# Kernel optimization log

Hardware: AMD Instinct MI355X
Metric: run time of the kernel (lower is better)

## Reference

```python
import jax, jax.numpy as jnp
import numpy as np

BATCH, SEQ, IN, HID = 64, 2048, 512, 512


def setup_inputs() -> dict:
    key = jax.random.key(0)
    ks = jax.random.split(key, 6)
    s = 1.0 / np.sqrt(HID)  # torch RNNCell uniform init scale
    return {
        "inputs": jax.random.normal(ks[0], (BATCH, SEQ, IN), dtype=jnp.float32),
        "h0": jax.random.normal(ks[1], (BATCH, HID), dtype=jnp.float32),
        "W_ih": jax.random.uniform(ks[2], (HID, IN), jnp.float32, -s, s),
        "W_hh": jax.random.uniform(ks[3], (HID, HID), jnp.float32, -s, s),
        "b_ih": jax.random.uniform(ks[4], (HID,), jnp.float32, -s, s),
        "b_hh": jax.random.uniform(ks[5], (HID,), jnp.float32, -s, s),
    }


def reference(inputs, h0, W_ih, W_hh, b_ih, b_hh):
    # hidden_state.reshape(-1, hidden_size) in the original
    h0 = h0.reshape(-1, W_hh.shape[0])
    # Precompute input projection for all timesteps in one big GEMM: [B,S,H]
    x_proj = jnp.einsum("bsi,hi->bsh", inputs, W_ih) + b_ih

    def step(h, xp_t):  # xp_t: [B,H]
        h_new = jnp.tanh(xp_t + h @ W_hh.T + b_hh)
        return h_new, h_new

    h_final, outs = jax.lax.scan(step, h0, jnp.swapaxes(x_proj, 0, 1))
    return jnp.swapaxes(outs, 0, 1), h_final  # ([B,S,H], [B,H])
```

## Files before the change

kernel.cpp:

```cpp
#include <hip/hip_runtime.h>

#define B_ 64
#define S_ 2048
#define I_ 512
#define H_ 512

typedef _Float16 half2v __attribute__((ext_vector_type(2)));
typedef _Float16 half8v __attribute__((ext_vector_type(8)));
typedef float    float4v __attribute__((ext_vector_type(4)));
typedef unsigned int uint4v __attribute__((ext_vector_type(4)));
typedef unsigned short ushort_t;

__device__ inline unsigned int pk2(float a, float b) {
    return __builtin_bit_cast(unsigned int, __builtin_amdgcn_cvt_pkrtz(a, b));
}

__device__ inline uint4v pack8(float4v a, float4v b) {
    uint4v r;
    r.x = pk2(a.x, a.y);
    r.y = pk2(a.z, a.w);
    r.z = pk2(b.x, b.y);
    r.w = pk2(b.z, b.w);
    return r;
}

__device__ inline float fdot2u(unsigned int h2, unsigned int w2, float acc) {
    return __builtin_amdgcn_fdot2(__builtin_bit_cast(half2v, h2),
                                  __builtin_bit_cast(half2v, w2), acc, false);
}

__global__ __launch_bounds__(256, 2) void xproj_gemm(
    const float* __restrict__ A,
    const float* __restrict__ Bw,
    const float* __restrict__ bias,
    float* __restrict__ C)
{
    __shared__ uint4v As[64 * 5];
    __shared__ uint4v Bs[512 * 5];

    const int tid  = threadIdx.x;
    const int wave = tid >> 6;
    const int lane = tid & 63;
    const int lm   = lane & 15;
    const int lq   = lane >> 4;
    const int m0   = blockIdx.x * 64;
    const int nb   = wave * 128;

    float4v acc[4][8];
#pragma unroll
    for (int mf = 0; mf < 4; ++mf)
#pragma unroll
        for (int nf = 0; nf < 8; ++nf)
            acc[mf][nf] = (float4v){0.f, 0.f, 0.f, 0.f};

    float biasv[8];
#pragma unroll
    for (int nf = 0; nf < 8; ++nf)
        biasv[nf] = bias[nb + nf * 16 + lm];

    const int sm    = tid >> 2;
    const int skq   = tid & 3;
    const int sslot = skq ^ (sm & 3);

    for (int kt = 0; kt < 16; ++kt) {
        const int k0 = kt * 32;
        const float* ap = A + (size_t)(m0 + sm) * 512 + k0 + skq * 8;
        float4v a0 = *(const float4v*)ap;
        float4v a1 = *(const float4v*)(ap + 4);
        float4v b0[8], b1[8];
#pragma unroll
        for (int i = 0; i < 8; ++i) {
            const float* bp = Bw + (size_t)(sm + 64 * i) * 512 + k0 + skq * 8;
            b0[i] = *(const float4v*)bp;
            b1[i] = *(const float4v*)(bp + 4);
        }
        __syncthreads();
        As[sm * 5 + sslot] = pack8(a0, a1);
#pragma unroll
        for (int i = 0; i < 8; ++i)
            Bs[(sm + 64 * i) * 5 + sslot] = pack8(b0[i], b1[i]);
        __syncthreads();

        half8v af[4];
#pragma unroll
        for (int mf = 0; mf < 4; ++mf) {
            int row = mf * 16 + lm;
            af[mf] = __builtin_bit_cast(half8v, As[row * 5 + (lq ^ (lm & 3))]);
        }
        half8v bfr[8];
#pragma unroll
        for (int nf = 0; nf < 8; ++nf) {
            int row = nb + nf * 16 + lm;
            bfr[nf] = __builtin_bit_cast(half8v, Bs[row * 5 + (lq ^ (lm & 3))]);
        }
#pragma unroll
        for (int mf = 0; mf < 4; ++mf)
#pragma unroll
            for (int nf = 0; nf < 8; ++nf)
                acc[mf][nf] = __builtin_amdgcn_mfma_f32_16x16x32_f16(
                    af[mf], bfr[nf], acc[mf][nf], 0, 0, 0);
    }

#pragma unroll
    for (int mf = 0; mf < 4; ++mf) {
        int mrow = m0 + mf * 16 + lq * 4;
#pragma unroll
        for (int nf = 0; nf < 8; ++nf) {
            float* cp = C + (size_t)mrow * 512 + nb + nf * 16 + lm;
            float4v v = acc[mf][nf];
            cp[0]    = v.x + biasv[nf];
            cp[512]  = v.y + biasv[nf];
            cp[1024] = v.z + biasv[nf];
            cp[1536] = v.w + biasv[nf];
        }
    }
}

__global__ __launch_bounds__(1024, 1) void rnn_scan(
    const float* __restrict__ h0,
    const float* __restrict__ Whh,
    const float* __restrict__ bhh,
    float* __restrict__ out)
{
    __shared__ uint4v stagev[2][64];
    __shared__ float  part[512];

    const int tid = threadIdx.x;
    const int j   = tid & 511;
    const int kh  = tid >> 9;
    const int b   = blockIdx.x;

    unsigned int w[128];
    const float* wp = Whh + (size_t)j * 512 + kh * 256;
#pragma unroll
    for (int c = 0; c < 64; ++c) {
        float4v f = *(const float4v*)(wp + c * 4);
        w[c * 2 + 0] = pk2(f.x, f.y);
        w[c * 2 + 1] = pk2(f.z, f.w);
    }

    float bj = 0.f, xpA = 0.f, xpB = 0.f;
    float* outb = out + (size_t)b * S_ * H_ + j;
    if (kh == 0) {
        ((ushort_t*)stagev)[j] = (ushort_t)pk2(h0[b * 512 + j], 0.f);
        bj  = bhh[j];
        xpA = outb[0];
        xpB = outb[512];
    }
    __syncthreads();

    for (int t = 0; t < S_; ++t) {
        const uint4v* hs = &stagev[t & 1][kh * 32];
        float a0 = 0.f, a1 = 0.f, a2 = 0.f, a3 = 0.f;
#pragma unroll
        for (int c = 0; c < 32; ++c) {
            uint4v hh = hs[c];
            a0 = fdot2u(hh.x, w[c * 4 + 0], a0);
            a1 = fdot2u(hh.y, w[c * 4 + 1], a1);
            a2 = fdot2u(hh.z, w[c * 4 + 2], a2);
            a3 = fdot2u(hh.w, w[c * 4 + 3], a3);
        }
        float a = (a0 + a1) + (a2 + a3);
        if (kh == 1) part[j] = a;
        __syncthreads();
        if (kh == 0) {
            float y = a + part[j] + ((t & 1) ? xpB : xpA) + bj;
            float e = __builtin_amdgcn_exp2f(y * 2.88539008f);
            float h = 1.f - 2.f * __builtin_amdgcn_rcpf(e + 1.f);
            outb[(size_t)t * H_] = h;
            ((ushort_t*)stagev)[((t + 1) & 1) * 512 + j] = (ushort_t)pk2(h, 0.f);
            float nxt = outb[(size_t)(t + 2) * H_];
            if (t & 1) xpB = nxt; else xpA = nxt;
            if (t == S_ - 1) out[(size_t)B_ * S_ * H_ + b * 512 + j] = h;
        }
        __syncthreads();
    }
}

extern "C" void kernel_launch(void* const* d_in, const int* in_sizes, int n_in,
                              void* d_out, int out_size, void* d_ws, size_t ws_size,
                              hipStream_t stream) {
    const float* inputs = (const float*)d_in[0];
    const float* h0     = (const float*)d_in[1];
    const float* W_ih   = (const float*)d_in[2];
    const float* W_hh   = (const float*)d_in[3];
    const float* b_ih   = (const float*)d_in[4];
    const float* b_hh   = (const float*)d_in[5];
    float* out = (float*)d_out;

    hipLaunchKernelGGL(xproj_gemm, dim3(131072 / 64), dim3(256), 0, stream,
                       inputs, W_ih, b_ih, out);
    hipLaunchKernelGGL(rnn_scan, dim3(B_), dim3(1024), 0, stream,
                       h0, W_hh, b_hh, out);
}
```

Before: 6.836 ms.

## Restructure RNN scan into per-wave row groups with DPP reductions and single barrier

Each wave now owns 32 hidden rows, and each lane holds a K-slice of 8 rows of W_hh in registers. Partial dot products are reduced across lanes with DPP adds instead of a shared-memory partial buffer. This cuts the per-step barriers from two to one and unrolls the step loop by two to ping-pong the h buffers. Only 4 of every 16 lanes apply tanh and write two outputs each, which adds cross-lane reduction cost and selection logic per step.

```diff
diff --git a/kernel.cpp b/kernel.cpp
--- a/kernel.cpp
+++ b/kernel.cpp
@@ -8,6 +8,7 @@
 typedef _Float16 half2v __attribute__((ext_vector_type(2)));
 typedef _Float16 half8v __attribute__((ext_vector_type(8)));
 typedef float    float4v __attribute__((ext_vector_type(4)));
+typedef float    float2v __attribute__((ext_vector_type(2)));
 typedef unsigned int uint4v __attribute__((ext_vector_type(4)));
 typedef unsigned short ushort_t;
 
@@ -28,6 +29,15 @@
     return __builtin_amdgcn_fdot2(__builtin_bit_cast(half2v, h2),
                                   __builtin_bit_cast(half2v, w2), acc, false);
 }
+
+__device__ inline float fast_tanh(float y) {
+    float e = __builtin_amdgcn_exp2f(y * 2.88539008f);
+    return 1.f - 2.f * __builtin_amdgcn_rcpf(e + 1.f);
+}
+
+#define DPPADD(v, ctrl)                                                       \
+    ((v) + __builtin_bit_cast(float, __builtin_amdgcn_update_dpp(             \
+               0, __builtin_bit_cast(int, (v)), (ctrl), 0xf, 0xf, true)))
 
 __global__ __launch_bounds__(256, 2) void xproj_gemm(
     const float* __restrict__ A,
@@ -122,59 +132,108 @@
     const float* __restrict__ bhh,
     float* __restrict__ out)
 {
-    __shared__ uint4v stagev[2][64];
-    __shared__ float  part[512];
-
-    const int tid = threadIdx.x;
-    const int j   = tid & 511;
-    const int kh  = tid >> 9;
-    const int b   = blockIdx.x;
-
-    unsigned int w[128];
-    const float* wp = Whh + (size_t)j * 512 + kh * 256;
-#pragma unroll
-    for (int c = 0; c < 64; ++c) {
-        float4v f = *(const float4v*)(wp + c * 4);
-        w[c * 2 + 0] = pk2(f.x, f.y);
-        w[c * 2 + 1] = pk2(f.z, f.w);
-    }
-
-    float bj = 0.f, xpA = 0.f, xpB = 0.f;
-    float* outb = out + (size_t)b * S_ * H_ + j;
-    if (kh == 0) {
-        ((ushort_t*)stagev)[j] = (ushort_t)pk2(h0[b * 512 + j], 0.f);
-        bj  = bhh[j];
-        xpA = outb[0];
-        xpB = outb[512];
-    }
+    __shared__ uint4v stage0[64];
+    __shared__ uint4v stage1[64];
+
+    const int tid   = threadIdx.x;
+    const int w     = tid >> 6;
+    const int lane  = tid & 63;
+    const int jl    = lane >> 4;
+    const int kl    = lane & 15;
+    const int b     = blockIdx.x;
+    const int wbase = w * 32;
+
+    uint4v wf[8][4];
+#pragma unroll
+    for (int q = 0; q < 8; ++q) {
+        const float* wp = Whh + (size_t)(wbase + jl * 8 + q) * 512 + kl * 8;
+#pragma unroll
+        for (int i = 0; i < 4; ++i) {
+            float4v f0 = *(const float4v*)(wp + i * 128);
+            float4v f1 = *(const float4v*)(wp + i * 128 + 4);
+            wf[q][i] = pack8(f0, f1);
+        }
+    }
+
+    float* outb = out + (size_t)b * S_ * H_;
+    const int jj = wbase + jl * 8 + 2 * kl;
+
+    float be = 0.f, bo = 0.f;
+    float xeA = 0.f, xoA = 0.f, xeB = 0.f, xoB = 0.f;
+    if (kl < 4) {
+        be = bhh[jj];
+        bo = bhh[jj + 1];
+        float2v x0 = *(const float2v*)(outb + jj);
+        float2v x1 = *(const float2v*)(outb + H_ + jj);
+        xeA = x0.x; xoA = x0.y;
+        xeB = x1.x; xoB = x1.y;
+    }
+    if (tid < 512)
+        ((ushort_t*)stage0)[tid] = (ushort_t)pk2(h0[b * 512 + tid], 0.f);
     __syncthreads();
 
-    for (int t = 0; t < S_; ++t) {
-        const uint4v* hs = &stagev[t & 1][kh * 32];
-        float a0 = 0.f, a1 = 0.f, a2 = 0.f, a3 = 0.f;
-#pragma unroll
-        for (int c = 0; c < 32; ++c) {
-            uint4v hh = hs[c];
-            a0 = fdot2u(hh.x, w[c * 4 + 0], a0);
-            a1 = fdot2u(hh.y, w[c * 4 + 1], a1);
-            a2 = fdot2u(hh.z, w[c * 4 + 2], a2);
-            a3 = fdot2u(hh.w, w[c * 4 + 3], a3);
-        }
-        float a = (a0 + a1) + (a2 + a3);
-        if (kh == 1) part[j] = a;
-        __syncthreads();
-        if (kh == 0) {
-            float y = a + part[j] + ((t & 1) ? xpB : xpA) + bj;
-            float e = __builtin_amdgcn_exp2f(y * 2.88539008f);
-            float h = 1.f - 2.f * __builtin_amdgcn_rcpf(e + 1.f);
-            outb[(size_t)t * H_] = h;
-            ((ushort_t*)stagev)[((t + 1) & 1) * 512 + j] = (ushort_t)pk2(h, 0.f);
-            float nxt = outb[(size_t)(t + 2) * H_];
-            if (t & 1) xpB = nxt; else xpA = nxt;
-            if (t == S_ - 1) out[(size_t)B_ * S_ * H_ + b * 512 + j] = h;
-        }
-        __syncthreads();
-    }
+#define STEP(T, RBUF, WBUF, XE, XO)                                           \
+    {                                                                         \
+        uint4v hv0 = RBUF[kl];                                                \
+        uint4v hv1 = RBUF[16 + kl];                                           \
+        uint4v hv2 = RBUF[32 + kl];                                           \
+        uint4v hv3 = RBUF[48 + kl];                                           \
+        float acc[8];                                                         \
+        _Pragma("unroll") for (int q = 0; q < 8; ++q) {                       \
+            float a = 0.f;                                                    \
+            a = fdot2u(hv0.x, wf[q][0].x, a);                                 \
+            a = fdot2u(hv0.y, wf[q][0].y, a);                                 \
+            a = fdot2u(hv0.z, wf[q][0].z, a);                                 \
+            a = fdot2u(hv0.w, wf[q][0].w, a);                                 \
+            a = fdot2u(hv1.x, wf[q][1].x, a);                                 \
+            a = fdot2u(hv1.y, wf[q][1].y, a);                                 \
+            a = fdot2u(hv1.z, wf[q][1].z, a);                                 \
+            a = fdot2u(hv1.w, wf[q][1].w, a);                                 \
+            a = fdot2u(hv2.x, wf[q][2].x, a);                                 \
+            a = fdot2u(hv2.y, wf[q][2].y, a);                                 \
+            a = fdot2u(hv2.z, wf[q][2].z, a);                                 \
+            a = fdot2u(hv2.w, wf[q][2].w, a);                                 \
+            a = fdot2u(hv3.x, wf[q][3].x, a);                                 \
+            a = fdot2u(hv3.y, wf[q][3].y, a);                                 \
+            a = fdot2u(hv3.z, wf[q][3].z, a);                                 \
+            a = fdot2u(hv3.w, wf[q][3].w, a);                                 \
+            acc[q] = a;                                                       \
+        }                                                                     \
+        _Pragma("unroll") for (int q = 0; q < 8; ++q) {                       \
+            float v = acc[q];                                                 \
+            v = DPPADD(v, 0xB1);             \
+            v = DPPADD(v, 0x4E);             \
+            v = DPPADD(v, 0x124);                              \
+            v = DPPADD(v, 0x128);                              \
+            acc[q] = v;                                                       \
+        }                                                                     \
+        if (kl < 4) {                                                         \
+            float ea = (kl & 1) ? acc[2] : acc[0];                            \
+            float eb = (kl & 1) ? acc[6] : acc[4];                            \
+            float oa = (kl & 1) ? acc[3] : acc[1];                            \
+            float ob = (kl & 1) ? acc[7] : acc[5];                            \
+            float ye = (kl & 2) ? eb : ea;                                    \
+            float yo = (kl & 2) ? ob : oa;                                    \
+            ye = fast_tanh(ye + (XE) + be);                                   \
+            yo = fast_tanh(yo + (XO) + bo);                                   \
+            *(float2v*)(outb + (size_t)(T) * H_ + jj) = (float2v){ye, yo};    \
+            ((unsigned int*)(WBUF))[jj >> 1] = pk2(ye, yo);                   \
+            \
+            \
+            float2v xn = *(const float2v*)(outb + (size_t)((T) + 2) * H_ + jj);\
+            (XE) = xn.x; (XO) = xn.y;                                         \
+            if ((T) == S_ - 1)                                                \
+                *(float2v*)(out + (size_t)B_ * S_ * H_ + b * H_ + jj) =       \
+                    (float2v){ye, yo};                                        \
+        }                                                                     \
+        __syncthreads();                                                      \
+    }
+
+    for (int t = 0; t < S_; t += 2) {
+        STEP(t,     stage0, stage1, xeA, xoA);
+        STEP(t + 1, stage1, stage0, xeB, xoB);
+    }
+#undef STEP
 }
 
 extern "C" void kernel_launch(void* const* d_in, const int* in_sizes, int n_in,
```

After: 8.786 ms. +28.5%, slower.

## Split each batch row's recurrence across four workgroups with flag-based cross-block sync

Applied to the files above, without the earlier changes.

The scan kernel now assigns each batch element to four cooperating workgroups, each owning 128 hidden units. This uses 256 blocks instead of 64 and cuts the per-block weight slice and dot-product chain length. Each block publishes its new hidden slice to global memory and signals a release flag. It then spins on the other three blocks' flags, gathers their slices into LDS and starts the next step. Partial sums are reduced with DPP lane rotations instead of an LDS partial buffer. This adds a global-memory round trip and a spin-wait per timestep, and correctness relies on all 256 blocks being co-resident.

```diff
diff --git a/kernel.cpp b/kernel.cpp
--- a/kernel.cpp
+++ b/kernel.cpp
@@ -8,6 +8,7 @@
 typedef _Float16 half2v __attribute__((ext_vector_type(2)));
 typedef _Float16 half8v __attribute__((ext_vector_type(8)));
 typedef float    float4v __attribute__((ext_vector_type(4)));
+typedef float    float2v __attribute__((ext_vector_type(2)));
 typedef unsigned int uint4v __attribute__((ext_vector_type(4)));
 typedef unsigned short ushort_t;
 
@@ -27,6 +28,28 @@
 __device__ inline float fdot2u(unsigned int h2, unsigned int w2, float acc) {
     return __builtin_amdgcn_fdot2(__builtin_bit_cast(half2v, h2),
                                   __builtin_bit_cast(half2v, w2), acc, false);
+}
+
+__device__ inline float fast_tanh(float y) {
+    float e = __builtin_amdgcn_exp2f(y * 2.88539008f);
+    return 1.f - 2.f * __builtin_amdgcn_rcpf(e + 1.f);
+}
+
+#define DPPADD(v, ctrl)                                                       \
+    ((v) + __builtin_bit_cast(float, __builtin_amdgcn_update_dpp(             \
+               0, __builtin_bit_cast(int, (v)), (ctrl), 0xf, 0xf, true)))
+#define DPPMOV(v, ctrl)                                                       \
+    (__builtin_bit_cast(float, __builtin_amdgcn_update_dpp(                   \
+        0, __builtin_bit_cast(int, (v)), (ctrl), 0xf, 0xf, true)))
+
+__device__ inline int swz(int w) {
+    int sw = w >> 4;
+    int i4 = (w >> 2) & 3;
+    return sw * 16 + ((i4 ^ ((sw >> 1) & 3)) * 4) + (w & 3);
+}
+
+__global__ void zero_flags(int* __restrict__ flags) {
+    flags[threadIdx.x] = 0;
 }
 
 __global__ __launch_bounds__(256, 2) void xproj_gemm(
@@ -116,62 +139,127 @@
     }
 }
 
-__global__ __launch_bounds__(1024, 1) void rnn_scan(
+__global__ __launch_bounds__(512, 1) void rnn_scan4(
     const float* __restrict__ h0,
     const float* __restrict__ Whh,
     const float* __restrict__ bhh,
-    float* __restrict__ out)
+    float* __restrict__ out,
+    int* __restrict__ flags)
 {
-    __shared__ uint4v stagev[2][64];
-    __shared__ float  part[512];
+    __shared__ unsigned int hw[2 * 256];
 
     const int tid = threadIdx.x;
-    const int j   = tid & 511;
-    const int kh  = tid >> 9;
-    const int b   = blockIdx.x;
-
-    unsigned int w[128];
-    const float* wp = Whh + (size_t)j * 512 + kh * 256;
-#pragma unroll
-    for (int c = 0; c < 64; ++c) {
-        float4v f = *(const float4v*)(wp + c * 4);
-        w[c * 2 + 0] = pk2(f.x, f.y);
-        w[c * 2 + 1] = pk2(f.z, f.w);
-    }
-
-    float bj = 0.f, xpA = 0.f, xpB = 0.f;
-    float* outb = out + (size_t)b * S_ * H_ + j;
-    if (kh == 0) {
-        ((ushort_t*)stagev)[j] = (ushort_t)pk2(h0[b * 512 + j], 0.f);
-        bj  = bhh[j];
-        xpA = outb[0];
-        xpB = outb[512];
+    const int l   = tid & 63;
+    const int w8  = tid >> 6;
+    const int jlo = l & 3;
+    const int kh  = (l >> 2) & 3;
+    const int jhi = l >> 4;
+    const int bid = blockIdx.x;
+    const int b   = bid & 63;
+    const int c   = bid >> 6;
+
+    const int jloc = w8 * 16 + jhi * 4;
+    const int jg   = c * 128 + jloc + jlo;
+    const int s    = kh * 4 + jlo;
+    const int X    = (s >> 1) & 3;
+
+    uint4v wv[4][4];
+#pragma unroll
+    for (int p = 0; p < 4; ++p) {
+        const float* wr =
+            Whh + (size_t)(c * 128 + jloc + ((jlo + p) & 3)) * 512 + s * 32;
+#pragma unroll
+        for (int i = 0; i < 4; ++i) {
+            const float* wp = wr + (i ^ X) * 8;
+            float4v f0 = *(const float4v*)wp;
+            float4v f1 = *(const float4v*)(wp + 4);
+            wv[p][i] = pack8(f0, f1);
+        }
+    }
+
+    float* outb = out + (size_t)b * (S_ * H_);
+    const float bj = bhh[jg];
+    float xpA = outb[jg];
+    float xpB = outb[H_ + jg];
+
+    if (tid < 256) {
+        float f0 = h0[b * 512 + 2 * tid];
+        float f1 = h0[b * 512 + 2 * tid + 1];
+        hw[swz(tid)] = pk2(f0, f1);
     }
     __syncthreads();
 
     for (int t = 0; t < S_; ++t) {
-        const uint4v* hs = &stagev[t & 1][kh * 32];
-        float a0 = 0.f, a1 = 0.f, a2 = 0.f, a3 = 0.f;
-#pragma unroll
-        for (int c = 0; c < 32; ++c) {
-            uint4v hh = hs[c];
-            a0 = fdot2u(hh.x, w[c * 4 + 0], a0);
-            a1 = fdot2u(hh.y, w[c * 4 + 1], a1);
-            a2 = fdot2u(hh.z, w[c * 4 + 2], a2);
-            a3 = fdot2u(hh.w, w[c * 4 + 3], a3);
-        }
-        float a = (a0 + a1) + (a2 + a3);
-        if (kh == 1) part[j] = a;
-        __syncthreads();
-        if (kh == 0) {
-            float y = a + part[j] + ((t & 1) ? xpB : xpA) + bj;
-            float e = __builtin_amdgcn_exp2f(y * 2.88539008f);
-            float h = 1.f - 2.f * __builtin_amdgcn_rcpf(e + 1.f);
-            outb[(size_t)t * H_] = h;
-            ((ushort_t*)stagev)[((t + 1) & 1) * 512 + j] = (ushort_t)pk2(h, 0.f);
-            float nxt = outb[(size_t)(t + 2) * H_];
+        const uint4v* hb = (const uint4v*)(hw + (t & 1) * 256);
+        uint4v t0 = hb[s * 4 + 0];
+        uint4v t1 = hb[s * 4 + 1];
+        uint4v t2 = hb[s * 4 + 2];
+        uint4v t3 = hb[s * 4 + 3];
+
+        float acc = 0.f;
+#pragma unroll
+        for (int p = 0; p < 4; ++p) {
+            acc = fdot2u(t0.x, wv[p][0].x, acc);
+            acc = fdot2u(t0.y, wv[p][0].y, acc);
+            acc = fdot2u(t0.z, wv[p][0].z, acc);
+            acc = fdot2u(t0.w, wv[p][0].w, acc);
+            acc = fdot2u(t1.x, wv[p][1].x, acc);
+            acc = fdot2u(t1.y, wv[p][1].y, acc);
+            acc = fdot2u(t1.z, wv[p][1].z, acc);
+            acc = fdot2u(t1.w, wv[p][1].w, acc);
+            acc = fdot2u(t2.x, wv[p][2].x, acc);
+            acc = fdot2u(t2.y, wv[p][2].y, acc);
+            acc = fdot2u(t2.z, wv[p][2].z, acc);
+            acc = fdot2u(t2.w, wv[p][2].w, acc);
+            acc = fdot2u(t3.x, wv[p][3].x, acc);
+            acc = fdot2u(t3.y, wv[p][3].y, acc);
+            acc = fdot2u(t3.z, wv[p][3].z, acc);
+            acc = fdot2u(t3.w, wv[p][3].w, acc);
+            acc = DPPMOV(acc, 0x39);
+        }
+        acc = DPPADD(acc, 0x124);
+        acc = DPPADD(acc, 0x128);
+
+        const float xp = (t & 1) ? xpB : xpA;
+        const float h  = fast_tanh(acc + xp + bj);
+
+        if (kh == 0)
+            __hip_atomic_store((int*)(outb + (size_t)t * H_ + jg),
+                               __builtin_bit_cast(int, h),
+                               __ATOMIC_RELAXED, __HIP_MEMORY_SCOPE_AGENT);
+        {
+            float nxt = outb[(size_t)(t + 2) * H_ + jg];
             if (t & 1) xpB = nxt; else xpA = nxt;
-            if (t == S_ - 1) out[(size_t)B_ * S_ * H_ + b * 512 + j] = h;
+        }
+        if (t == S_ - 1 && kh == 0)
+            out[(size_t)B_ * S_ * H_ + b * H_ + jg] = h;
+
+        __syncthreads();
+        if (tid == 60)
+            __hip_atomic_store(&flags[b * 4 + c], t + 1,
+                               __ATOMIC_RELEASE, __HIP_MEMORY_SCOPE_AGENT);
+        if (t == S_ - 1) break;
+
+        if (tid < 3) {
+            const int pp = (c + 1 + tid) & 3;
+            while (__hip_atomic_load(&flags[b * 4 + pp], __ATOMIC_ACQUIRE,
+                                     __HIP_MEMORY_SCOPE_AGENT) < t + 1)
+                __builtin_amdgcn_s_sleep(1);
+        }
+        __syncthreads();
+
+        unsigned int* hd = hw + ((t + 1) & 1) * 256;
+        float hq = DPPMOV(h, 0xB1);
+        if (kh == 0 && (jlo & 1) == 0)
+            hd[swz(jg >> 1)] = pk2(h, hq);
+        if (tid < 192) {
+            int w  = tid + (tid >= c * 64 ? 64 : 0);
+            int i0 = __hip_atomic_load((const int*)(outb + (size_t)t * H_ + 2 * w),
+                                       __ATOMIC_RELAXED, __HIP_MEMORY_SCOPE_AGENT);
+            int i1 = __hip_atomic_load((const int*)(outb + (size_t)t * H_ + 2 * w + 1),
+                                       __ATOMIC_RELAXED, __HIP_MEMORY_SCOPE_AGENT);
+            hd[swz(w)] = pk2(__builtin_bit_cast(float, i0),
+                             __builtin_bit_cast(float, i1));
         }
         __syncthreads();
     }
@@ -187,9 +275,11 @@
     const float* b_ih   = (const float*)d_in[4];
     const float* b_hh   = (const float*)d_in[5];
     float* out = (float*)d_out;
-
+    int* flags = (int*)d_ws;
+
+    hipLaunchKernelGGL(zero_flags, dim3(1), dim3(256), 0, stream, flags);
     hipLaunchKernelGGL(xproj_gemm, dim3(131072 / 64), dim3(256), 0, stream,
                        inputs, W_ih, b_ih, out);
-    hipLaunchKernelGGL(rnn_scan, dim3(B_), dim3(1024), 0, stream,
-                       h0, W_hh, b_hh, out);
-}
+    hipLaunchKernelGGL(rnn_scan4, dim3(256), dim3(512), 0, stream,
+                       h0, W_hh, b_hh, out, flags);
+}
```

Result: slower. 12.71 ms (+86.0%).

## Restructure recurrent scan into 512-thread blocks with AGPR/LDS-resident weights and DPP rotation

Applied to the files above, without the earlier changes.

Rewrites the recurrent scan kernel to use 512 threads per batch instead of 1024. Each thread holds three quarters of its W_hh slice as fp16 in accumulator registers and the remaining quarter in LDS. The dot product is split across 16-lane groups, and partial sums rotate between lanes with DPP row-rotate moves, which removes the cross-half partial-sum exchange and one barrier per step. The new hidden state is packed in pairs via a DPP swap into a swizzled LDS buffer. The cost is more complex register and LDS traffic, with AGPR reads and LDS weight loads added on every step.

```diff
diff --git a/kernel.cpp b/kernel.cpp
--- a/kernel.cpp
+++ b/kernel.cpp
@@ -9,7 +9,6 @@
 typedef _Float16 half8v __attribute__((ext_vector_type(8)));
 typedef float    float4v __attribute__((ext_vector_type(4)));
 typedef unsigned int uint4v __attribute__((ext_vector_type(4)));
-typedef unsigned short ushort_t;
 
 __device__ inline unsigned int pk2(float a, float b) {
     return __builtin_bit_cast(unsigned int, __builtin_amdgcn_cvt_pkrtz(a, b));
@@ -28,6 +27,15 @@
     return __builtin_amdgcn_fdot2(__builtin_bit_cast(half2v, h2),
                                   __builtin_bit_cast(half2v, w2), acc, false);
 }
+
+__device__ inline float fast_tanh(float y) {
+    float e = __builtin_amdgcn_exp2f(y * 2.88539008f);
+    return 1.f - 2.f * __builtin_amdgcn_rcpf(e + 1.f);
+}
+
+#define DPPMOVF(v, ctrl)                                                      \
+    (__builtin_bit_cast(float, __builtin_amdgcn_update_dpp(                   \
+        0, __builtin_bit_cast(int, (v)), (ctrl), 0xf, 0xf, true)))
 
 __global__ __launch_bounds__(256, 2) void xproj_gemm(
     const float* __restrict__ A,
@@ -116,63 +124,114 @@
     }
 }
 
-__global__ __launch_bounds__(1024, 1) void rnn_scan(
+__global__ __launch_bounds__(512, 1) void rnn_scan_agpr(
     const float* __restrict__ h0,
     const float* __restrict__ Whh,
     const float* __restrict__ bhh,
     float* __restrict__ out)
 {
-    __shared__ uint4v stagev[2][64];
-    __shared__ float  part[512];
+    __shared__ unsigned int hbuf[2][256];
+    __shared__ uint4v wlds[16 * 8 * 64];
 
     const int tid = threadIdx.x;
-    const int j   = tid & 511;
-    const int kh  = tid >> 9;
+    const int l   = tid & 63;
+    const int w8  = tid >> 6;
+    const int lam = l & 15;
+    const int r   = l >> 4;
     const int b   = blockIdx.x;
-
-    unsigned int w[128];
-    const float* wp = Whh + (size_t)j * 512 + kh * 256;
-#pragma unroll
-    for (int c = 0; c < 64; ++c) {
-        float4v f = *(const float4v*)(wp + c * 4);
-        w[c * 2 + 0] = pk2(f.x, f.y);
-        w[c * 2 + 1] = pk2(f.z, f.w);
-    }
-
-    float bj = 0.f, xpA = 0.f, xpB = 0.f;
-    float* outb = out + (size_t)b * S_ * H_ + j;
-    if (kh == 0) {
-        ((ushort_t*)stagev)[j] = (ushort_t)pk2(h0[b * 512 + j], 0.f);
-        bj  = bhh[j];
-        xpA = outb[0];
-        xpB = outb[512];
-    }
+    const int jb  = w8 * 64 + r * 16;
+
+    int rv = __builtin_amdgcn_update_dpp(0, lam, 0x121, 0xf, 0xf, true);
+    const int sgn = (rv == ((lam + 15) & 15)) ? 15 : 1;
+
+    unsigned int wa[192];
+#pragma unroll
+    for (int p = 0; p < 12; ++p) {
+        const float* wr =
+            Whh + (size_t)(jb + ((lam + sgn * p) & 15)) * 512 + 32 * lam;
+#pragma unroll
+        for (int uu = 0; uu < 8; ++uu) {
+            float4v f = *(const float4v*)(wr + 4 * uu);
+            unsigned int v0 = pk2(f.x, f.y);
+            unsigned int v1 = pk2(f.z, f.w);
+            asm volatile("v_accvgpr_write_b32 %0, %1"
+                         : "=a"(wa[p * 16 + 2 * uu]) : "v"(v0));
+            asm volatile("v_accvgpr_write_b32 %0, %1"
+                         : "=a"(wa[p * 16 + 2 * uu + 1]) : "v"(v1));
+        }
+    }
+
+#pragma unroll
+    for (int q = 0; q < 4; ++q) {
+        const float* wr =
+            Whh + (size_t)(jb + ((lam + sgn * (12 + q)) & 15)) * 512 + 32 * lam;
+#pragma unroll
+        for (int i = 0; i < 4; ++i) {
+            float4v f0 = *(const float4v*)(wr + 8 * i);
+            float4v f1 = *(const float4v*)(wr + 8 * i + 4);
+            wlds[((q * 4 + i) * 8 + w8) * 64 + l] = pack8(f0, f1);
+        }
+    }
+
+    if (tid < 256) {
+        int k2 = tid;
+        float f0 = h0[b * 512 + 2 * k2];
+        float f1 = h0[b * 512 + 2 * k2 + 1];
+        hbuf[0][((k2 >> 2) & 3) * 64 + (k2 >> 4) * 4 + (k2 & 3)] = pk2(f0, f1);
+    }
+
+    const float bj = bhh[tid];
+    float* outb = out + (size_t)b * (S_ * H_);
+    float xpA = outb[tid];
+    float xpB = outb[H_ + tid];
     __syncthreads();
 
     for (int t = 0; t < S_; ++t) {
-        const uint4v* hs = &stagev[t & 1][kh * 32];
-        float a0 = 0.f, a1 = 0.f, a2 = 0.f, a3 = 0.f;
-#pragma unroll
-        for (int c = 0; c < 32; ++c) {
-            uint4v hh = hs[c];
-            a0 = fdot2u(hh.x, w[c * 4 + 0], a0);
-            a1 = fdot2u(hh.y, w[c * 4 + 1], a1);
-            a2 = fdot2u(hh.z, w[c * 4 + 2], a2);
-            a3 = fdot2u(hh.w, w[c * 4 + 3], a3);
-        }
-        float a = (a0 + a1) + (a2 + a3);
-        if (kh == 1) part[j] = a;
-        __syncthreads();
-        if (kh == 0) {
-            float y = a + part[j] + ((t & 1) ? xpB : xpA) + bj;
-            float e = __builtin_amdgcn_exp2f(y * 2.88539008f);
-            float h = 1.f - 2.f * __builtin_amdgcn_rcpf(e + 1.f);
-            outb[(size_t)t * H_] = h;
-            ((ushort_t*)stagev)[((t + 1) & 1) * 512 + j] = (ushort_t)pk2(h, 0.f);
-            float nxt = outb[(size_t)(t + 2) * H_];
-            if (t & 1) xpB = nxt; else xpA = nxt;
-            if (t == S_ - 1) out[(size_t)B_ * S_ * H_ + b * 512 + j] = h;
-        }
+        const uint4v* hb4 = (const uint4v*)&hbuf[t & 1][0];
+        uint4v h4[4];
+#pragma unroll
+        for (int i4 = 0; i4 < 4; ++i4)
+            h4[i4] = hb4[i4 * 16 + lam];
+
+        float acc = 0.f;
+#pragma unroll
+        for (int p = 0; p < 12; ++p) {
+#pragma unroll
+            for (int u = 0; u < 16; ++u) {
+                unsigned int wt;
+                asm volatile("v_accvgpr_read_b32 %0, %1"
+                             : "=v"(wt) : "a"(wa[p * 16 + u]));
+                acc = fdot2u(h4[u >> 2][u & 3], wt, acc);
+            }
+            acc = DPPMOVF(acc, 0x121);
+        }
+#pragma unroll
+        for (int q = 0; q < 4; ++q) {
+            uint4v wq[4];
+#pragma unroll
+            for (int i = 0; i < 4; ++i)
+                wq[i] = wlds[((q * 4 + i) * 8 + w8) * 64 + l];
+#pragma unroll
+            for (int u = 0; u < 16; ++u)
+                acc = fdot2u(h4[u >> 2][u & 3], wq[u >> 2][u & 3], acc);
+            acc = DPPMOVF(acc, 0x121);
+        }
+
+        const float xp = (t & 1) ? xpB : xpA;
+        const float h  = fast_tanh(acc + xp + bj);
+
+        outb[(size_t)t * H_ + tid] = h;
+        float hq = DPPMOVF(h, 0xB1);
+        if ((tid & 1) == 0) {
+            int k2 = tid >> 1;
+            hbuf[(t + 1) & 1][((k2 >> 2) & 3) * 64 + (k2 >> 4) * 4 + (k2 & 3)] =
+                pk2(h, hq);
+        }
+        float nxt = outb[(size_t)(t + 2) * H_ + tid];
+        if (t & 1) xpB = nxt; else xpA = nxt;
+        if (t == S_ - 1)
+            out[(size_t)B_ * S_ * H_ + b * H_ + tid] = h;
+
         __syncthreads();
     }
 }
@@ -187,9 +246,10 @@
     const float* b_ih   = (const float*)d_in[4];
     const float* b_hh   = (const float*)d_in[5];
     float* out = (float*)d_out;
+    (void)d_ws; (void)ws_size;
 
     hipLaunchKernelGGL(xproj_gemm, dim3(131072 / 64), dim3(256), 0, stream,
                        inputs, W_ih, b_ih, out);
-    hipLaunchKernelGGL(rnn_scan, dim3(B_), dim3(1024), 0, stream,
+    hipLaunchKernelGGL(rnn_scan_agpr, dim3(B_), dim3(512), 0, stream,
                        h0, W_hh, b_hh, out);
 }
```

After: 5.950 ms. 1.15x faster.
